# Kernel optimization log

Hardware: AMD Instinct MI355X
Metric: run time of the kernel (lower is better)

Reference implementation:

```python
import jax, jax.numpy as jnp
from jax import lax
import numpy as np

STRIDE = 16.0
PRE_NMS_TOPN = 2000
POST_NMS_TOPN = 300
NMS_THRESH = 0.7
BBOX_XFORM_CLIP = float(np.log(1000.0 / 16.0))
NUM_ANCHORS = 15

# ---- Detectron generate_anchors (numpy, done once) ----

def _whctrs(a):
    w = a[2] - a[0] + 1.0
    h = a[3] - a[1] + 1.0
    return w, h, a[0] + 0.5 * (w - 1), a[1] + 0.5 * (h - 1)

def _mkanchors(ws, hs, xc, yc):
    ws = ws[:, None]; hs = hs[:, None]
    return np.hstack([xc - 0.5 * (ws - 1), yc - 0.5 * (hs - 1),
                      xc + 0.5 * (ws - 1), yc + 0.5 * (hs - 1)])

def _ratio_enum(anchor, ratios):
    w, h, xc, yc = _whctrs(anchor)
    size = w * h
    ws = np.round(np.sqrt(size / ratios))
    hs = np.round(ws * ratios)
    return _mkanchors(ws, hs, xc, yc)

def _scale_enum(anchor, scales):
    w, h, xc, yc = _whctrs(anchor)
    return _mkanchors(w * scales, h * scales, xc, yc)

def generate_anchors(stride, sizes, ratios):
    base = np.array([1, 1, stride, stride], dtype=np.float64) - 1
    ra = _ratio_enum(base, np.asarray(ratios, np.float64))
    anchors = np.vstack([_scale_enum(ra[i], np.asarray(sizes, np.float64) / stride)
                         for i in range(ra.shape[0])])
    return anchors.astype(np.float32)

ANCHORS_NP = generate_anchors(STRIDE, (32, 64, 128, 256, 512), (0.5, 1.0, 2.0))

# ---- proposal helpers (jax) ----

def decode_boxes(anchors, deltas):
    w = anchors[:, 2] - anchors[:, 0] + 1.0
    h = anchors[:, 3] - anchors[:, 1] + 1.0
    cx = anchors[:, 0] + 0.5 * w
    cy = anchors[:, 1] + 0.5 * h
    dx, dy = deltas[:, 0], deltas[:, 1]
    dw = jnp.minimum(deltas[:, 2], BBOX_XFORM_CLIP)
    dh = jnp.minimum(deltas[:, 3], BBOX_XFORM_CLIP)
    pcx = dx * w + cx
    pcy = dy * h + cy
    pw = jnp.exp(dw) * w
    ph = jnp.exp(dh) * h
    return jnp.stack([pcx - 0.5 * pw, pcy - 0.5 * ph,
                      pcx + 0.5 * pw - 1.0, pcy + 0.5 * ph - 1.0], axis=-1)

def clip_boxes(b, info):
    hmax = info[0] - 1.0
    wmax = info[1] - 1.0
    return jnp.stack([jnp.clip(b[:, 0], 0.0, wmax), jnp.clip(b[:, 1], 0.0, hmax),
                      jnp.clip(b[:, 2], 0.0, wmax), jnp.clip(b[:, 3], 0.0, hmax)], axis=-1)

def nms_keep(boxes):
    # boxes already sorted by descending score; greedy NMS via scan
    x1, y1, x2, y2 = boxes[:, 0], boxes[:, 1], boxes[:, 2], boxes[:, 3]
    areas = (x2 - x1 + 1.0) * (y2 - y1 + 1.0)
    xx1 = jnp.maximum(x1[:, None], x1[None, :])
    yy1 = jnp.maximum(y1[:, None], y1[None, :])
    xx2 = jnp.minimum(x2[:, None], x2[None, :])
    yy2 = jnp.minimum(y2[:, None], y2[None, :])
    inter = jnp.maximum(xx2 - xx1 + 1.0, 0.0) * jnp.maximum(yy2 - yy1 + 1.0, 0.0)
    iou = inter / (areas[:, None] + areas[None, :] - inter)
    K = boxes.shape[0]

    def body(keep, i):
        sup = jnp.any(keep & (iou[i] > NMS_THRESH))
        keep = keep.at[i].set(~sup)
        return keep, None

    keep, _ = lax.scan(body, jnp.zeros((K,), bool), jnp.arange(K))
    return keep


def setup_inputs() -> dict:
    key = jax.random.key(0)
    ks = jax.random.split(key, 4)
    x = jax.random.normal(ks[0], (2, 1024, 50, 84), jnp.float32)
    conv_w = 0.01 * jax.random.normal(ks[1], (1024, 1024, 3, 3), jnp.float32)
    conv_b = jnp.zeros((1024,), jnp.float32)
    cls_w = 0.01 * jax.random.normal(ks[2], (2 * NUM_ANCHORS, 1024, 1, 1), jnp.float32)
    cls_b = jnp.zeros((2 * NUM_ANCHORS,), jnp.float32)
    bbox_w = 0.01 * jax.random.normal(ks[3], (4 * NUM_ANCHORS, 1024, 1, 1), jnp.float32)
    bbox_b = jnp.zeros((4 * NUM_ANCHORS,), jnp.float32)
    im_info = jnp.array([[800.0, 1344.0, 1.0], [800.0, 1344.0, 1.0]], jnp.float32)
    return {"x": x, "conv_w": conv_w, "conv_b": conv_b, "cls_w": cls_w,
            "cls_b": cls_b, "bbox_w": bbox_w, "bbox_b": bbox_b, "im_info": im_info}


def reference(x, conv_w, conv_b, cls_w, cls_b, bbox_w, bbox_b, im_info):
    A = NUM_ANCHORS
    anchors = jnp.asarray(ANCHORS_NP)
    dn = ('NCHW', 'OIHW', 'NCHW')
    h = jax.nn.relu(lax.conv_general_dilated(x, conv_w, (1, 1), 'SAME',
                                             dimension_numbers=dn) + conv_b[None, :, None, None])
    cls_logits = lax.conv_general_dilated(h, cls_w, (1, 1), 'VALID',
                                          dimension_numbers=dn) + cls_b[None, :, None, None]
    bbox_pred = lax.conv_general_dilated(h, bbox_w, (1, 1), 'VALID',
                                         dimension_numbers=dn) + bbox_b[None, :, None, None]
    B, _, H, W = cls_logits.shape
    # softmax over the 2-way fg/bg axis, take fg prob: [B, A, H, W]
    prob = jax.nn.softmax(cls_logits.reshape(B, 2, A, H, W), axis=1)[:, 1]
    scores = prob.transpose(0, 2, 3, 1).reshape(B, -1)               # [B, H*W*A]
    deltas = bbox_pred.transpose(0, 2, 3, 1).reshape(B, H * W * A, 4)
    # shifted anchor grid, (h, w, a) flatten order matching Detectron
    sy = jnp.arange(H, dtype=jnp.float32) * STRIDE
    sx = jnp.arange(W, dtype=jnp.float32) * STRIDE
    ys, xs = jnp.meshgrid(sy, sx, indexing='ij')
    shifts = jnp.stack([xs, ys, xs, ys], axis=-1).reshape(-1, 4)      # [H*W, 4]
    all_anchors = (shifts[:, None, :] + anchors[None, :, :]).reshape(-1, 4)

    def per_image(sc, dl, info):
        boxes = clip_boxes(decode_boxes(all_anchors, dl), info)
        top_sc, idx = lax.top_k(sc, PRE_NMS_TOPN)
        top_boxes = boxes[idx]
        keep = nms_keep(top_boxes)
        order = jnp.argsort((~keep).astype(jnp.int32))[:POST_NMS_TOPN]  # kept first, score order
        valid = keep[order]
        out_boxes = jnp.where(valid[:, None], top_boxes[order], 0.0)
        out_sc = jnp.where(valid, top_sc[order], 0.0)
        return out_boxes, out_sc

    rois_b, probs_b = jax.vmap(per_image)(scores, deltas, im_info)
    batch_ids = jnp.repeat(jnp.arange(B, dtype=jnp.float32), POST_NMS_TOPN)
    rois = jnp.concatenate([batch_ids[:, None], rois_b.reshape(-1, 4)], axis=1)
    return cls_logits, bbox_pred, rois, probs_b.reshape(-1, 1)
```

## Files before the change

kernel.cpp:

```cpp
#include <hip/hip_runtime.h>
#include <math.h>

#define BATCH   2
#define CIN     1024
#define COUT    1024
#define HH      50
#define WW      84
#define HWX     4200
#define NA      15
#define NSC     63000
#define TOPN    2000
#define POSTN   300
#define CAPG    8192
#define CLS_OFF   0
#define BBOX_OFF  252000
#define ROIS_OFF  756000
#define PROBS_OFF 759000

#define TPI 273
#define USTR 274

__constant__ double ANCH[NA][4] = {
  {-15.0,  -4.0,  30.0, 19.0},
  {-38.0, -16.0,  53.0, 31.0},
  {-84.0, -40.0,  99.0, 55.0},
  {-176.0,-88.0, 191.0,103.0},
  {-360.0,-184.0,375.0,199.0},
  {-8.0,  -8.0,  23.0, 23.0},
  {-24.0, -24.0, 39.0, 39.0},
  {-56.0, -56.0, 71.0, 71.0},
  {-120.0,-120.0,135.0,135.0},
  {-248.0,-248.0,263.0,263.0},
  {-3.0, -14.0, 18.0, 29.0},
  {-14.0, -36.0, 29.0, 51.0},
  {-36.0, -80.0, 51.0, 95.0},
  {-80.0,-168.0, 95.0,183.0},
  {-168.0,-344.0,183.0,359.0}
};

__constant__ double BTd[6][6] = {
  {4.0,  0.0, -5.0,  0.0, 1.0, 0.0},
  {0.0, -4.0, -4.0,  1.0, 1.0, 0.0},
  {0.0,  4.0, -4.0, -1.0, 1.0, 0.0},
  {0.0, -2.0, -1.0,  2.0, 1.0, 0.0},
  {0.0,  2.0, -1.0, -2.0, 1.0, 0.0},
  {0.0,  4.0,  0.0, -5.0, 0.0, 1.0}
};
__constant__ double ATd[4][6] = {
  {1.0, 1.0,  1.0, 1.0,  1.0, 0.0},
  {0.0, 1.0, -1.0, 2.0, -2.0, 0.0},
  {0.0, 1.0,  1.0, 4.0,  4.0, 0.0},
  {0.0, 1.0, -1.0, 8.0, -8.0, 1.0}
};

#define BBOX_CLIP 4.1351665567423560

#define WS_WT     0
#define WS_U      98304
#define WS_V      3465216
#define WS_C      16048128
#define WS_H64    19402752
#define OV_H      WS_V
#define OV_SC     (WS_C + 0)
#define OV_TIDX   (WS_C + 126000)
#define OV_TSC    (WS_C + 130000)
#define OV_BOX    (WS_C + 134000)
#define OV_MASK   (WS_C + 166000)
#define OV_GH     (WS_C + 422000)
#define OV_GH2    (OV_GH  + 512)
#define OV_GCA    (OV_GH2 + 512)
#define OV_GCB    (OV_GCA + 16)
#define OV_GCN    (OV_GCB + 16)
#define OV_GK     (OV_GCN + 16)
#define TZ_WORDS  (512 + 512 + 16 + 16 + 16 + 32768)

typedef double dx4 __attribute__((ext_vector_type(4)));

__device__ __forceinline__ void gload16(const void* gptr, void* lptr) {
  __builtin_amdgcn_global_load_lds(
      (const __attribute__((address_space(1))) unsigned int*)gptr,
      (__attribute__((address_space(3))) unsigned int*)lptr, 16, 0, 0);
}
#define MFMA64(a, b, c) __builtin_amdgcn_mfma_f64_16x16x4f64(a, b, c, 0, 0, 0)

__launch_bounds__(256)
__global__ void itrans_k(const float* __restrict__ x, double* __restrict__ U,
                         int b, int r) {
  __shared__ float XT[8][6][84];
  const int bx = blockIdx.x;
  const int cg  = bx & 127;
  const int ty  = bx >> 7;
  const int ci0 = cg * 8;
  for (int e = threadIdx.x; e < 4032; e += 256) {
    int ci = e / 504, rem = e % 504;
    int ry = rem / 84, xx = rem % 84;
    int y = ty*4 - 1 + ry;
    float v = 0.f;
    if (y >= 0 && y < HH) v = x[((size_t)(b*CIN + ci0 + ci)*HH + y)*WW + xx];
    XT[ci][ry][xx] = v;
  }
  __syncthreads();
  const int tid = threadIdx.x;
  if (tid < 168) {
    const int ci = tid / 21, tx = tid % 21;
    const double c0 = BTd[r][0], c1 = BTd[r][1], c2 = BTd[r][2];
    const double c3 = BTd[r][3], c4 = BTd[r][4], c5 = BTd[r][5];
    double tt[6];
#pragma unroll
    for (int j = 0; j < 6; ++j) {
      int col = tx*4 - 1 + j;
      double v = 0.0;
      if (col >= 0 && col < WW) {
        v = c0*(double)XT[ci][0][col] + c1*(double)XT[ci][1][col]
          + c2*(double)XT[ci][2][col] + c3*(double)XT[ci][3][col]
          + c4*(double)XT[ci][4][col] + c5*(double)XT[ci][5][col];
      }
      tt[j] = v;
    }
    const int t = ty*21 + tx;
#pragma unroll
    for (int c = 0; c < 6; ++c) {
      double u = BTd[c][0]*tt[0] + BTd[c][1]*tt[1] + BTd[c][2]*tt[2]
               + BTd[c][3]*tt[3] + BTd[c][4]*tt[4] + BTd[c][5]*tt[5];
      U[(size_t)(c*1024 + ci0 + ci)*USTR + t] = u;
    }
  }
}

#define GR0(a,b,c) (0.25*(a))
#define GR1(a,b,c) (-((a)+(b)+(c))*(1.0/6.0))
#define GR2(a,b,c) ((-(a)+(b)-(c))*(1.0/6.0))
#define GR3(a,b,c) (((a)+2.0*(b)+4.0*(c))*(1.0/24.0))
#define GR4(a,b,c) (((a)-2.0*(b)+4.0*(c))*(1.0/24.0))
#define GR5(a,b,c) ((c))
__launch_bounds__(256)
__global__ void wtrans_k(const float* __restrict__ conv_w, double* __restrict__ V,
                         int r) {
  const int g = blockIdx.x*256 + threadIdx.x;
  const int co = g & 1023, ci = g >> 10;
  const float* gp = conv_w + (size_t)(co*1024 + ci)*9;
  double g00 = (double)gp[0], g01 = (double)gp[1], g02 = (double)gp[2];
  double g10 = (double)gp[3], g11 = (double)gp[4], g12 = (double)gp[5];
  double g20 = (double)gp[6], g21 = (double)gp[7], g22 = (double)gp[8];
  double p0, p1, p2;
  switch (r) {
    case 0: p0=GR0(g00,g10,g20); p1=GR0(g01,g11,g21); p2=GR0(g02,g12,g22); break;
    case 1: p0=GR1(g00,g10,g20); p1=GR1(g01,g11,g21); p2=GR1(g02,g12,g22); break;
    case 2: p0=GR2(g00,g10,g20); p1=GR2(g01,g11,g21); p2=GR2(g02,g12,g22); break;
    case 3: p0=GR3(g00,g10,g20); p1=GR3(g01,g11,g21); p2=GR3(g02,g12,g22); break;
    case 4: p0=GR4(g00,g10,g20); p1=GR4(g01,g11,g21); p2=GR4(g02,g12,g22); break;
    default:p0=GR5(g00,g10,g20); p1=GR5(g01,g11,g21); p2=GR5(g02,g12,g22); break;
  }
  const size_t cico = (size_t)ci*1024 + co;
  V[0ull*1048576ull + cico] = GR0(p0,p1,p2);
  V[1ull*1048576ull + cico] = GR1(p0,p1,p2);
  V[2ull*1048576ull + cico] = GR2(p0,p1,p2);
  V[3ull*1048576ull + cico] = GR3(p0,p1,p2);
  V[4ull*1048576ull + cico] = GR4(p0,p1,p2);
  V[5ull*1048576ull + cico] = GR5(p0,p1,p2);
}

__launch_bounds__(256, 2)
__global__ void wgemm_k(const double* __restrict__ U, const double* __restrict__ V,
                        double* __restrict__ C) {
  __shared__ __align__(16) double As[2][32*64];
  __shared__ __align__(16) double Bs[2][32*64];
  const int tid = threadIdx.x;
  const int lane = tid & 63;
  const int w = tid >> 6;
  const int wm = w >> 1, wn = w & 1;
  const int l15 = lane & 15, lq = lane >> 4;
  const int bx = blockIdx.x;
  const int mt = bx >> 4, nt = bx & 15;
  const int t0 = mt * 64, n0 = nt * 64;
  const int z = blockIdx.z;
  const double* Ub = U + (size_t)z * (1024ull*USTR);
  const double* Vb = V + (size_t)z * 1048576ull;
  double* Cb = C + (size_t)z * ((size_t)TPI*1024);

  int pidx[4], nidx[4];
  {
    dx4 pr = {0.,0.,0.,0.}, pc = {0.,0.,0.,0.};
    pr = MFMA64((double)l15, 1.0, pr);
    pc = MFMA64(1.0, (double)l15, pc);
#pragma unroll
    for (int i = 0; i < 4; ++i) {
      pidx[i] = ((int)pr[i]) >> 2;
      nidx[i] = ((int)pc[i]) >> 2;
    }
  }

  auto stage = [&](int k0s, int slot) {
    char* Ad = (char*)&As[slot][0];
    char* Bd = (char*)&Bs[slot][0];
#pragma unroll
    for (int i = 0; i < 4; ++i) {
      int u = tid + i*256;
      int row = u >> 5, cp = u & 31;
      int t = t0 + 2*cp; if (t > 272) t = 272;
      gload16(Ub + (size_t)(k0s + row)*USTR + t, Ad + u*16);
    }
#pragma unroll
    for (int i = 0; i < 4; ++i) {
      int u = tid + i*256;
      int row = u >> 5, cp = u & 31;
      gload16(Vb + (size_t)(k0s + row)*1024 + n0 + 2*cp, Bd + u*16);
    }
  };

  dx4 acc[2][2];
#pragma unroll
  for (int i = 0; i < 2; ++i)
#pragma unroll
    for (int j = 0; j < 2; ++j) acc[i][j] = (dx4){0.,0.,0.,0.};

  stage(0, 0);
  __syncthreads();
  int cur = 0;
#pragma unroll 1
  for (int k0 = 0; k0 < 1024; k0 += 32) {
    if (k0 + 32 < 1024) stage(k0 + 32, cur ^ 1);
    const double* Ap = &As[cur][0];
    const double* Bp = &Bs[cur][0];
#pragma unroll
    for (int kk = 0; kk < 32; kk += 4) {
      const int ar = (kk + lq)*64 + wm*32 + l15;
      double a0 = Ap[ar], a1 = Ap[ar + 16];
      const int br = (kk + lq)*64 + wn*32 + l15;
      double b0 = Bp[br], b1 = Bp[br + 16];
      acc[0][0] = MFMA64(a0, b0, acc[0][0]);
      acc[0][1] = MFMA64(a0, b1, acc[0][1]);
      acc[1][0] = MFMA64(a1, b0, acc[1][0]);
      acc[1][1] = MFMA64(a1, b1, acc[1][1]);
    }
    __syncthreads();
    cur ^= 1;
  }

#pragma unroll
  for (int m2 = 0; m2 < 2; ++m2) {
#pragma unroll
    for (int n2 = 0; n2 < 2; ++n2) {
#pragma unroll
      for (int i = 0; i < 4; ++i) {
        int t = t0 + wm*32 + m2*16 + pidx[i];
        int co = n0 + wn*32 + n2*16 + nidx[i];
        if (t < TPI) Cb[(size_t)t*1024 + co] = acc[m2][n2][i];
      }
    }
  }
}

__launch_bounds__(256)
__global__ void otrans_k(const double* __restrict__ C, double* __restrict__ h64b,
                         int r) {
  const int g = blockIdx.x*256 + threadIdx.x;
  const int co = g & 1023, t = g >> 10;
  double m0 = C[((size_t)0*TPI + t)*1024 + co];
  double m1 = C[((size_t)1*TPI + t)*1024 + co];
  double m2 = C[((size_t)2*TPI + t)*1024 + co];
  double m3 = C[((size_t)3*TPI + t)*1024 + co];
  double m4 = C[((size_t)4*TPI + t)*1024 + co];
  double m5 = C[((size_t)5*TPI + t)*1024 + co];
  double s[4];
#pragma unroll
  for (int bb = 0; bb < 4; ++bb)
    s[bb] = ATd[bb][0]*m0 + ATd[bb][1]*m1 + ATd[bb][2]*m2
          + ATd[bb][3]*m3 + ATd[bb][4]*m4 + ATd[bb][5]*m5;
  const int ty = t / 21, tx = t % 21;
#pragma unroll
  for (int a = 0; a < 4; ++a) {
    const int y = ty*4 + a;
    if (y >= HH) continue;
    const double fa = ATd[a][r];
#pragma unroll
    for (int bb = 0; bb < 4; ++bb) {
      const size_t idx = ((size_t)(y*WW + tx*4 + bb))*1024 + co;
      if (r == 0) h64b[idx] = fa * s[bb];
      else        h64b[idx] += fa * s[bb];
    }
  }
}

__launch_bounds__(256)
__global__ void fin_k(const double* __restrict__ h64, const float* __restrict__ bias,
                      float* __restrict__ h) {
  __shared__ float T[64*65];
  const int m0  = blockIdx.x * 64;
  const int co0 = blockIdx.y * 64;
  const int b   = blockIdx.z;
  const int tid = threadIdx.x;
#pragma unroll
  for (int i = 0; i < 16; ++i) {
    int e = tid + i*256;
    int mi = e >> 6, coi = e & 63;
    int m = m0 + mi;
    double v = 0.0;
    if (m < HWX) v = h64[((size_t)b*HWX + m)*1024 + co0 + coi];
    T[mi*65 + coi] = (float)fmax(v + (double)bias[co0 + coi], 0.0);
  }
  __syncthreads();
#pragma unroll
  for (int i = 0; i < 16; ++i) {
    int e = tid + i*256;
    int coi = e >> 6, mi = e & 63;
    int m = m0 + mi;
    if (m < HWX) h[((size_t)(b*COUT + co0 + coi))*HWX + m] = T[mi*65 + coi];
  }
}

__global__ void wt_k(const float* __restrict__ cls_w, const float* __restrict__ bbox_w,
                     float* __restrict__ wT) {
  int t = blockIdx.x*256 + threadIdx.x;
  if (t >= 96*1024) return;
  int c = t / 96, o = t - (t/96)*96;
  float v = 0.f;
  if (o < 30)      v = cls_w[(size_t)o*1024 + c];
  else if (o < 90) v = bbox_w[(size_t)(o-30)*1024 + c];
  wT[t] = v;
}

__launch_bounds__(256, 2)
__global__ void heads_k(const float* __restrict__ h, const float* __restrict__ wT,
                        const float* __restrict__ cls_b, const float* __restrict__ bbox_b,
                        float* __restrict__ out_cls, float* __restrict__ out_bbox) {
  __shared__ __align__(16) float As[2][32*32];
  __shared__ __align__(16) float Bs[2][32*96];
  const int tid = threadIdx.x;
  const int lane = tid & 63;
  const int w = tid >> 6;
  const int wm = w >> 1, wn = w & 1;
  const int l15 = lane & 15, lq = lane >> 4;
  const int mt = blockIdx.x, b = blockIdx.y;
  const int m0 = mt * 32;

  int pidx[4], nidx[4];
  {
    dx4 pr = {0.,0.,0.,0.}, pc = {0.,0.,0.,0.};
    pr = MFMA64((double)l15, 1.0, pr);
    pc = MFMA64(1.0, (double)l15, pc);
#pragma unroll
    for (int i = 0; i < 4; ++i) {
      pidx[i] = ((int)pr[i]) >> 2;
      nidx[i] = ((int)pc[i]) >> 2;
    }
  }

  auto stage = [&](int c0, int slot) {
    {
      int row = tid >> 3, cp = tid & 7;
      int mm = m0 + cp*4; if (mm > HWX - 4) mm = HWX - 4;
      gload16(h + ((size_t)(b*COUT + c0 + row))*HWX + mm,
              (char*)&As[slot][0] + tid*16);
    }
#pragma unroll
    for (int i = 0; i < 3; ++i) {
      int e = tid + i*256;
      int row = e / 24, q = e % 24;
      gload16(wT + (size_t)(c0 + row)*96 + q*4,
              (char*)&Bs[slot][0] + e*16);
    }
  };

  dx4 acc[3];
#pragma unroll
  for (int j = 0; j < 3; ++j) acc[j] = (dx4){0.,0.,0.,0.};

  stage(0, 0);
  __syncthreads();
  int cur = 0;
#pragma unroll 1
  for (int c0 = 0; c0 < CIN; c0 += 32) {
    if (c0 + 32 < CIN) stage(c0 + 32, cur ^ 1);
    const float* Ap = &As[cur][0];
    const float* Bp = &Bs[cur][0];
#pragma unroll
    for (int kk = 0; kk < 32; kk += 4) {
      double a0 = (double)Ap[(kk + lq)*32 + wm*16 + l15];
      const int bb = (kk + lq)*96 + wn*48 + l15;
      double b0 = (double)Bp[bb];
      double b1 = (double)Bp[bb + 16];
      double b2 = (double)Bp[bb + 32];
      acc[0] = MFMA64(a0, b0, acc[0]);
      acc[1] = MFMA64(a0, b1, acc[1]);
      acc[2] = MFMA64(a0, b2, acc[2]);
    }
    __syncthreads();
    cur ^= 1;
  }

#pragma unroll
  for (int nf = 0; nf < 3; ++nf) {
#pragma unroll
    for (int i = 0; i < 4; ++i) {
      int m = m0 + wm*16 + pidx[i];
      int o = wn*48 + nf*16 + nidx[i];
      if (m < HWX) {
        if (o < 30) {
          out_cls[((size_t)(b*30 + o))*HWX + m] =
              (float)(acc[nf][i] + (double)cls_b[o]);
        } else if (o < 90) {
          out_bbox[((size_t)(b*60 + (o - 30)))*HWX + m] =
              (float)(acc[nf][i] + (double)bbox_b[o - 30]);
        }
      }
    }
  }
}

__global__ void score_k(const float* __restrict__ out_cls, float* __restrict__ scores) {
  int t = blockIdx.x*256 + threadIdx.x;
  if (t >= BATCH*NSC) return;
  int b = t / NSC; int r = t - b*NSC;
  int m = r / NA;  int a = r - m*NA;
  float l0 = out_cls[((size_t)(b*30 + a))*HWX + m];
  float l1 = out_cls[((size_t)(b*30 + a + NA))*HWX + m];
  double p = 1.0 / (1.0 + exp((double)l0 - (double)l1));
  scores[t] = (float)p;
}


__global__ void tz_k(unsigned* __restrict__ gz) {
  int t = blockIdx.x*256 + threadIdx.x;
  if (t < TZ_WORDS) gz[t] = 0u;
}

__launch_bounds__(256)
__global__ void histA_k(const float* __restrict__ scores, unsigned* __restrict__ ghist) {
  __shared__ unsigned lh[256];
  const int b = blockIdx.y;
  const int base = blockIdx.x * 1024;
  lh[threadIdx.x] = 0;
  __syncthreads();
  const float* sc = scores + (size_t)b*NSC;
#pragma unroll
  for (int q = 0; q < 4; ++q) {
    int i = base + threadIdx.x + q*256;
    if (i < NSC) atomicAdd(&lh[__float_as_uint(sc[i]) >> 24], 1u);
  }
  __syncthreads();
  unsigned v = lh[threadIdx.x];
  if (v) atomicAdd(&ghist[b*256 + threadIdx.x], v);
}

__launch_bounds__(256)
__global__ void cutA_k(const unsigned* __restrict__ ghist, unsigned* __restrict__ gcutA) {
  __shared__ unsigned s[256];
  const int b = blockIdx.x;
  const int t = threadIdx.x;
  s[t] = ghist[b*256 + t];
  __syncthreads();
  for (int off = 1; off < 256; off <<= 1) {
    unsigned v = (t + off < 256) ? s[t + off] : 0u;
    __syncthreads();
    s[t] += v;
    __syncthreads();
  }
  unsigned cum  = s[t];
  unsigned cum1 = (t < 255) ? s[t + 1] : 0u;
  if (cum >= TOPN && (t == 255 || cum1 < TOPN))
    gcutA[b] = ((unsigned)t << 16) | (TOPN - cum1);
}

__launch_bounds__(256)
__global__ void histB_k(const float* __restrict__ scores, const unsigned* __restrict__ gcutA,
                        unsigned* __restrict__ ghist2) {
  __shared__ unsigned lh[256];
  const int b = blockIdx.y;
  const unsigned b1 = gcutA[b] >> 16;
  const int base = blockIdx.x * 1024;
  lh[threadIdx.x] = 0;
  __syncthreads();
  const float* sc = scores + (size_t)b*NSC;
#pragma unroll
  for (int q = 0; q < 4; ++q) {
    int i = base + threadIdx.x + q*256;
    if (i < NSC) {
      unsigned k = __float_as_uint(sc[i]);
      if ((k >> 24) == b1) atomicAdd(&lh[(k >> 16) & 255u], 1u);
    }
  }
  __syncthreads();
  unsigned v = lh[threadIdx.x];
  if (v) atomicAdd(&ghist2[b*256 + threadIdx.x], v);
}

__launch_bounds__(256)
__global__ void cutB_k(const unsigned* __restrict__ ghist2, const unsigned* __restrict__ gcutA,
                       unsigned* __restrict__ gcutB) {
  __shared__ unsigned s[256];
  const int b = blockIdx.x;
  const int t = threadIdx.x;
  const unsigned b1 = gcutA[b] >> 16, need = gcutA[b] & 0xFFFFu;
  s[t] = ghist2[b*256 + t];
  __syncthreads();
  for (int off = 1; off < 256; off <<= 1) {
    unsigned v = (t + off < 256) ? s[t + off] : 0u;
    __syncthreads();
    s[t] += v;
    __syncthreads();
  }
  unsigned cum  = s[t];
  unsigned cum1 = (t < 255) ? s[t + 1] : 0u;
  if (cum >= need && (t == 255 || cum1 < need))
    gcutB[b] = (b1 << 8) | (unsigned)t;
}

__launch_bounds__(256)
__global__ void compact_k(const float* __restrict__ scores, const unsigned* __restrict__ gcutB,
                          unsigned long long* __restrict__ gkeys, unsigned* __restrict__ gcnt) {
  const int b = blockIdx.y;
  const unsigned cut = gcutB[b];
  const int base = blockIdx.x * 1024;
  const int lane = threadIdx.x & 63;
  const float* sc = scores + (size_t)b*NSC;
#pragma unroll
  for (int q = 0; q < 4; ++q) {
    int i = base + threadIdx.x + q*256;
    bool pred = false; unsigned k = 0u;
    if (i < NSC) { k = __float_as_uint(sc[i]); pred = ((k >> 16) >= cut); }
    unsigned long long m = __ballot(pred);
    if (m) {
      int leader = __ffsll((long long)m) - 1;
      unsigned bp = 0;
      if (lane == leader) bp = atomicAdd(&gcnt[b], (unsigned)__popcll(m));
      bp = __shfl(bp, leader);
      if (pred) {
        unsigned p = bp + (unsigned)__popcll(m & ((1ull << lane) - 1ull));
        if (p < CAPG)
          gkeys[(size_t)b*CAPG + p] =
              ((unsigned long long)k << 32) | (unsigned long long)(0xFFFFFFFFu - (unsigned)i);
      }
    }
  }
}

__launch_bounds__(1024)
__global__ void sortk_k(const unsigned long long* __restrict__ gkeys,
                        unsigned* __restrict__ top_idx, float* __restrict__ top_score) {
  __shared__ unsigned long long key[CAPG];
  const int b = blockIdx.x;
  const int tid = threadIdx.x;
  for (int i = tid; i < CAPG; i += 1024) key[i] = gkeys[(size_t)b*CAPG + i];
  __syncthreads();
  for (int k2 = 2; k2 <= CAPG; k2 <<= 1) {
    for (int j = k2 >> 1; j > 0; j >>= 1) {
      for (int i = tid; i < CAPG; i += 1024) {
        int p = i ^ j;
        if (p > i) {
          unsigned long long a = key[i], c = key[p];
          bool up = ((i & k2) == 0);
          if (up ? (a < c) : (a > c)) { key[i] = c; key[p] = a; }
        }
      }
      __syncthreads();
    }
  }
  for (int i = tid; i < TOPN; i += 1024) {
    unsigned long long kk = key[i];
    top_idx[(size_t)b*TOPN + i]   = 0xFFFFFFFFu - (unsigned)(kk & 0xFFFFFFFFull);
    top_score[(size_t)b*TOPN + i] = __uint_as_float((unsigned)(kk >> 32));
  }
}

__global__ void decode_k(const unsigned* __restrict__ top_idx,
                         const float* __restrict__ out_bbox,
                         const float* __restrict__ im_info,
                         double* __restrict__ boxesd) {
  int t = blockIdx.x*256 + threadIdx.x;
  if (t >= BATCH*TOPN) return;
  int b = t / TOPN;
  unsigned idx = top_idx[t];
  int a = idx % NA; int m = idx / NA;
  int yy = m / WW;  int xx = m - yy*WW;
  double sx = (double)xx * 16.0, sy = (double)yy * 16.0;
  double A0 = ANCH[a][0] + sx, A1 = ANCH[a][1] + sy;
  double A2 = ANCH[a][2] + sx, A3 = ANCH[a][3] + sy;
  double w_ = A2 - A0 + 1.0, h_ = A3 - A1 + 1.0;
  double cx = A0 + 0.5*w_,  cy = A1 + 0.5*h_;
  const float* bp = out_bbox + (size_t)b*60*HWX;
  double dx = (double)bp[(a*4+0)*HWX + m];
  double dy = (double)bp[(a*4+1)*HWX + m];
  double dw = fmin((double)bp[(a*4+2)*HWX + m], BBOX_CLIP);
  double dh = fmin((double)bp[(a*4+3)*HWX + m], BBOX_CLIP);
  double pcx = dx*w_ + cx, pcy = dy*h_ + cy;
  double pw = exp(dw)*w_,  ph = exp(dh)*h_;
  double x1 = pcx - 0.5*pw, y1 = pcy - 0.5*ph;
  double x2 = pcx + 0.5*pw - 1.0, y2 = pcy + 0.5*ph - 1.0;
  double hmax = (double)im_info[b*3+0] - 1.0;
  double wmax = (double)im_info[b*3+1] - 1.0;
  x1 = fmin(fmax(x1, 0.0), wmax); x2 = fmin(fmax(x2, 0.0), wmax);
  y1 = fmin(fmax(y1, 0.0), hmax); y2 = fmin(fmax(y2, 0.0), hmax);
  boxesd[(size_t)t*4+0] = x1; boxesd[(size_t)t*4+1] = y1;
  boxesd[(size_t)t*4+2] = x2; boxesd[(size_t)t*4+3] = y2;
}

__launch_bounds__(256)
__global__ void iou_k(const double* __restrict__ boxesd,
                      unsigned long long* __restrict__ mask) {
  __shared__ double BX[TOPN*4];
  const int b  = blockIdx.y;
  const int i0 = blockIdx.x * 8;
  const double* src = boxesd + (size_t)b*TOPN*4;
  for (int e = threadIdx.x; e < TOPN*4; e += 256) BX[e] = src[e];
  __syncthreads();
  const int il = threadIdx.x >> 5;
  const int w  = threadIdx.x & 31;
  const int i  = i0 + il;
  double x1 = BX[i*4+0], y1 = BX[i*4+1], x2 = BX[i*4+2], y2 = BX[i*4+3];
  double ai = (x2 - x1 + 1.0)*(y2 - y1 + 1.0);
  unsigned long long bits = 0ull;
  for (int jj = 0; jj < 64; ++jj) {
    int j = w*64 + jj;
    if (j >= TOPN) break;
    double bx1 = BX[j*4+0], by1 = BX[j*4+1], bx2 = BX[j*4+2], by2 = BX[j*4+3];
    double xx1 = fmax(x1, bx1), yy1 = fmax(y1, by1);
    double xx2 = fmin(x2, bx2), yy2 = fmin(y2, by2);
    double iw = fmax(xx2 - xx1 + 1.0, 0.0);
    double ih = fmax(yy2 - yy1 + 1.0, 0.0);
    double inter = iw * ih;
    double aj = (bx2 - bx1 + 1.0)*(by2 - by1 + 1.0);
    double iou = inter / (ai + aj - inter);
    if (iou > 0.7) bits |= (1ull << jj);
  }
  mask[((size_t)b*TOPN + i)*32 + w] = bits;
}

__launch_bounds__(256)
__global__ void nms_out_k(const unsigned long long* __restrict__ mask,
                          const double* __restrict__ boxesd,
                          const float* __restrict__ top_score,
                          float* __restrict__ rois, float* __restrict__ probs) {
  __shared__ unsigned long long MS[256*32];
  __shared__ int kept_idx[POSTN];
  __shared__ int s_cnt, s_done;
  const int b = blockIdx.x;
  const int tid = threadIdx.x;
  if (tid == 0) { s_done = 0; s_cnt = 0; }

  unsigned long long rem = 0ull;
  int cnt = 0;
  const int L = tid;

  for (int ch = 0; ch < 8; ++ch) {
    __syncthreads();
    if (s_done) break;
    const int base = ch * 256;
    for (int e = tid; e < 256*32; e += 256) {
      int row = base + (e >> 5);
      MS[e] = (row < TOPN) ? mask[((size_t)b*TOPN + row)*32 + (e & 31)] : 0ull;
    }
    __syncthreads();
    if (tid < 64) {
      const int lim = (base + 256 < TOPN) ? base + 256 : TOPN;
      int pos = base;
      while (true) {
        unsigned long long wmask = ~rem;
        int lo = pos - 64*L;
        if (lo >= 64) wmask = 0ull;
        else if (lo > 0) wmask &= (~0ull) << lo;
        int hi = lim - 64*L;
        if (hi <= 0) wmask = 0ull;
        else if (hi < 64) wmask &= ((1ull << hi) - 1ull);
        if (L >= 32) wmask = 0ull;
        unsigned long long bal = __ballot(wmask != 0ull);
        if (bal == 0ull) break;
        int lstar = __ffsll((long long)bal) - 1;
        int cand = 64*L + (wmask ? (__ffsll((long long)wmask) - 1) : 0);
        int i = __shfl(cand, lstar);
        if (L == 0) kept_idx[cnt] = i;
        ++cnt;
        if (cnt >= POSTN) {
          if (L == 0) { s_done = 1; }
          break;
        }
        if (L < 32) rem |= MS[(i - base)*32 + L];
        pos = i + 1;
      }
      if (L == 0) s_cnt = cnt;
    }
  }
  __syncthreads();
  const int n = s_cnt;

  for (int j = tid; j < POSTN; j += 256) {
    float* rr = rois + ((size_t)b*POSTN + j)*5;
    rr[0] = (float)b; rr[1] = 0.f; rr[2] = 0.f; rr[3] = 0.f; rr[4] = 0.f;
    probs[(size_t)b*POSTN + j] = 0.f;
  }
  for (int j = tid; j < n; j += 256) {
    int i = kept_idx[j];
    const double* bx = boxesd + ((size_t)b*TOPN + i)*4;
    float* rr = rois + ((size_t)b*POSTN + j)*5;
    rr[1] = (float)bx[0]; rr[2] = (float)bx[1];
    rr[3] = (float)bx[2]; rr[4] = (float)bx[3];
    probs[(size_t)b*POSTN + j] = top_score[(size_t)b*TOPN + i];
  }
}

extern "C" void kernel_launch(void* const* d_in, const int* in_sizes, int n_in,
                              void* d_out, int out_size, void* d_ws, size_t ws_size,
                              hipStream_t stream) {
  const float* x      = (const float*)d_in[0];
  const float* conv_w = (const float*)d_in[1];
  const float* conv_b = (const float*)d_in[2];
  const float* cls_w  = (const float*)d_in[3];
  const float* cls_b  = (const float*)d_in[4];
  const float* bbox_w = (const float*)d_in[5];
  const float* bbox_b = (const float*)d_in[6];
  const float* im_info= (const float*)d_in[7];

  float* out  = (float*)d_out;
  float* out_cls  = out + CLS_OFF;
  float* out_bbox = out + BBOX_OFF;
  float* rois     = out + ROIS_OFF;
  float* probs    = out + PROBS_OFF;

  float* wsf = (float*)d_ws;
  float*    wT      = wsf + WS_WT;
  double*   U       = (double*)(wsf + WS_U);
  double*   V       = (double*)(wsf + WS_V);
  double*   Cws     = (double*)(wsf + WS_C);
  double*   h64     = (double*)(wsf + WS_H64);
  float*    h       = wsf + OV_H;
  float*    scores  = wsf + OV_SC;
  unsigned* top_idx = (unsigned*)(wsf + OV_TIDX);
  float*    top_sc  = wsf + OV_TSC;
  double*   boxesd  = (double*)(wsf + OV_BOX);
  unsigned long long* mask = (unsigned long long*)(wsf + OV_MASK);
  unsigned* ghist   = (unsigned*)(wsf + OV_GH);
  unsigned* ghist2  = (unsigned*)(wsf + OV_GH2);
  unsigned* gcutA   = (unsigned*)(wsf + OV_GCA);
  unsigned* gcutB   = (unsigned*)(wsf + OV_GCB);
  unsigned* gcnt    = (unsigned*)(wsf + OV_GCN);
  unsigned long long* gkeys = (unsigned long long*)(wsf + OV_GK);

  wt_k<<<dim3((96*1024 + 255)/256), dim3(256), 0, stream>>>(cls_w, bbox_w, wT);
  for (int r = 0; r < 6; ++r) {
    wtrans_k<<<dim3(4096), dim3(256), 0, stream>>>(conv_w, V, r);
    for (int b = 0; b < 2; ++b) {
      itrans_k<<<dim3(1664), dim3(256), 0, stream>>>(x, U, b, r);
      wgemm_k<<<dim3(80, 1, 6), dim3(256), 0, stream>>>(U, V, Cws);
      otrans_k<<<dim3(1092), dim3(256), 0, stream>>>(Cws, h64 + (size_t)b*HWX*1024, r);
    }
  }
  fin_k<<<dim3(66, 16, 2), dim3(256), 0, stream>>>(h64, conv_b, h);
  heads_k<<<dim3(132, 2), dim3(256), 0, stream>>>(h, wT, cls_b, bbox_b, out_cls, out_bbox);
  tz_k<<<dim3((TZ_WORDS + 255)/256), dim3(256), 0, stream>>>(ghist);
  score_k<<<dim3((BATCH*NSC + 255)/256), dim3(256), 0, stream>>>(out_cls, scores);
  histA_k<<<dim3(62, 2), dim3(256), 0, stream>>>(scores, ghist);
  cutA_k<<<dim3(2), dim3(256), 0, stream>>>(ghist, gcutA);
  histB_k<<<dim3(62, 2), dim3(256), 0, stream>>>(scores, gcutA, ghist2);
  cutB_k<<<dim3(2), dim3(256), 0, stream>>>(ghist2, gcutA, gcutB);
  compact_k<<<dim3(62, 2), dim3(256), 0, stream>>>(scores, gcutB, gkeys, gcnt);
  sortk_k<<<dim3(2), dim3(1024), 0, stream>>>(gkeys, top_idx, top_sc);
  decode_k<<<dim3((BATCH*TOPN + 255)/256), dim3(256), 0, stream>>>(top_idx, out_bbox, im_info, boxesd);
  iou_k<<<dim3(TOPN/8, 2), dim3(256), 0, stream>>>(boxesd, mask);
  nms_out_k<<<dim3(2), dim3(256), 0, stream>>>(mask, boxesd, top_sc, rois, probs);
}
```

Before: 1.877 ms.

## Replace single-block bitonic sort with parallel rank-by-counting top-k selection

The two-block bitonic sort over an 8192-entry shared buffer is replaced by a multi-block rank kernel. Each thread computes its key's rank by counting larger keys among the compacted candidates, then scatters directly into the top-N output. Only the valid candidate count is processed, so the key buffer no longer needs zero-filling and the tz_k clear shrinks. The counting is O(n^2) and relies on keys being unique, which the index packed into each key guarantees.

```diff
diff --git a/kernel.cpp b/kernel.cpp
--- a/kernel.cpp
+++ b/kernel.cpp
@@ -72,7 +72,7 @@
 #define OV_GCB    (OV_GCA + 16)
 #define OV_GCN    (OV_GCB + 16)
 #define OV_GK     (OV_GCN + 16)
-#define TZ_WORDS  (512 + 512 + 16 + 16 + 16 + 32768)
+#define TZ_WORDS  (512 + 512 + 16 + 16 + 16)
 
 typedef double dx4 __attribute__((ext_vector_type(4)));
 
@@ -535,31 +535,34 @@
   }
 }
 
-__launch_bounds__(1024)
-__global__ void sortk_k(const unsigned long long* __restrict__ gkeys,
-                        unsigned* __restrict__ top_idx, float* __restrict__ top_score) {
-  __shared__ unsigned long long key[CAPG];
-  const int b = blockIdx.x;
-  const int tid = threadIdx.x;
-  for (int i = tid; i < CAPG; i += 1024) key[i] = gkeys[(size_t)b*CAPG + i];
-  __syncthreads();
-  for (int k2 = 2; k2 <= CAPG; k2 <<= 1) {
-    for (int j = k2 >> 1; j > 0; j >>= 1) {
-      for (int i = tid; i < CAPG; i += 1024) {
-        int p = i ^ j;
-        if (p > i) {
-          unsigned long long a = key[i], c = key[p];
-          bool up = ((i & k2) == 0);
-          if (up ? (a < c) : (a > c)) { key[i] = c; key[p] = a; }
-        }
-      }
-      __syncthreads();
-    }
-  }
-  for (int i = tid; i < TOPN; i += 1024) {
-    unsigned long long kk = key[i];
-    top_idx[(size_t)b*TOPN + i]   = 0xFFFFFFFFu - (unsigned)(kk & 0xFFFFFFFFull);
-    top_score[(size_t)b*TOPN + i] = __uint_as_float((unsigned)(kk >> 32));
+#define RCH 2048
+__launch_bounds__(256)
+__global__ void rank_k(const unsigned long long* __restrict__ gkeys,
+                       const unsigned* __restrict__ gcnt,
+                       unsigned* __restrict__ top_idx, float* __restrict__ top_score) {
+  __shared__ unsigned long long ks[RCH];
+  const int b = blockIdx.y;
+  int count = (int)gcnt[b]; if (count > CAPG) count = CAPG;
+  if (blockIdx.x * 256 >= count) return;
+  const unsigned long long* kb = gkeys + (size_t)b*CAPG;
+  const int cand = blockIdx.x*256 + threadIdx.x;
+  const bool act = (cand < count);
+  const unsigned long long mykey = act ? kb[cand] : 0ull;
+  int rank = 0;
+#pragma unroll 1
+  for (int c0 = 0; c0 < count; c0 += RCH) {
+    const int lim = (count - c0 < RCH) ? (count - c0) : RCH;
+    __syncthreads();
+    for (int j = threadIdx.x; j < lim; j += 256) ks[j] = kb[c0 + j];
+    __syncthreads();
+    if (act) {
+#pragma unroll 4
+      for (int j = 0; j < lim; ++j) rank += (ks[j] > mykey) ? 1 : 0;
+    }
+  }
+  if (act && rank < TOPN) {
+    top_idx[(size_t)b*TOPN + rank]   = 0xFFFFFFFFu - (unsigned)(mykey & 0xFFFFFFFFull);
+    top_score[(size_t)b*TOPN + rank] = __uint_as_float((unsigned)(mykey >> 32));
   }
 }
 
@@ -753,7 +756,7 @@
   histB_k<<<dim3(62, 2), dim3(256), 0, stream>>>(scores, gcutA, ghist2);
   cutB_k<<<dim3(2), dim3(256), 0, stream>>>(ghist2, gcutA, gcutB);
   compact_k<<<dim3(62, 2), dim3(256), 0, stream>>>(scores, gcutB, gkeys, gcnt);
-  sortk_k<<<dim3(2), dim3(1024), 0, stream>>>(gkeys, top_idx, top_sc);
+  rank_k<<<dim3(CAPG/256, 2), dim3(256), 0, stream>>>(gkeys, gcnt, top_idx, top_sc);
   decode_k<<<dim3((BATCH*TOPN + 255)/256), dim3(256), 0, stream>>>(top_idx, out_bbox, im_info, boxesd);
   iou_k<<<dim3(TOPN/8, 2), dim3(256), 0, stream>>>(boxesd, mask);
   nms_out_k<<<dim3(2), dim3(256), 0, stream>>>(mask, boxesd, top_sc, rois, probs);
```

New measurement: 1.793 ms. -4.5%, faster.
